# Performance work log

Hardware: AMD Instinct MI355X
Metric: run time of the kernel (lower is better)

Reference implementation:

```python
import jax, jax.numpy as jnp
import numpy as np

C_IN = 128
C_OUT = 128
N_EDGE_TYPE = 7
N_NODE_TYPE = 7
AVG_DEGREE = 7
NUMD = 524288                 # nodes at depth d (multiple of 8)
LNUMD = 32768                 # leaf nodes at depth d-1
NNUM_DM1 = LNUMD + NUMD // 8  # 98304 nodes at depth d-1
PREFIX = 16384                # nodes at depths < d-1 kept in x
N_TOTAL_X = PREFIX + LNUMD + NUMD   # 573440
N_CONV = PREFIX + NNUM_DM1          # 114688 nodes seen by GraphConv
N_EDGES = N_CONV * AVG_DEGREE       # 802816


def setup_inputs() -> dict:
    key = jax.random.key(0)
    ks = jax.random.split(key, 6)
    x = jax.random.normal(ks[0], (N_TOTAL_X, C_IN), dtype=jnp.float32)
    # exactly LNUMD True entries (98304 = 3 * 32768), deterministic
    leaf_mask = (jnp.arange(NNUM_DM1) % 3) == 0
    edge_index = jax.random.randint(ks[1], (2, N_EDGES), 0, N_CONV)
    edge_type = jax.random.randint(ks[2], (N_EDGES,), 0, N_EDGE_TYPE)
    node_type = jax.random.randint(ks[3], (N_CONV,), 0, N_NODE_TYPE)
    w_down = jax.random.normal(ks[4], (C_IN, C_IN, 8), dtype=jnp.float32) * 0.02
    w_conv = jax.random.normal(
        ks[5], (N_EDGE_TYPE * (C_IN + N_NODE_TYPE), C_OUT), dtype=jnp.float32) * 0.02
    return dict(x=x, leaf_mask=leaf_mask, edge_index=edge_index,
                edge_type=edge_type, node_type=node_type,
                w_down=w_down, w_conv=w_conv)


def _graph_conv(x, edge_index, edge_type, node_type, w_conv):
    # x: [N, C]; augment with one-hot node type (n_node_type > 1)
    one_hot = jax.nn.one_hot(node_type, N_NODE_TYPE, dtype=x.dtype)
    xa = jnp.concatenate([x, one_hot], axis=1)          # [N, C+T]
    row, col = edge_index[0], edge_index[1]
    bucket = row * N_EDGE_TYPE + edge_type              # [E]
    # scatter-add neighbor features into per-(node, edge_type) buckets
    col_data = jax.ops.segment_sum(xa[col], bucket,
                                   num_segments=x.shape[0] * N_EDGE_TYPE)
    # [N, n_edge_type*(C+T)] @ [n_edge_type*(C+T), C_out]
    return col_data.reshape(x.shape[0], -1) @ w_conv


def reference(x, leaf_mask, edge_index, edge_type, node_type, w_down, w_conv):
    # Downsample: merge groups of 8 child nodes with a (C, C*8) weight
    xd = x[-NUMD:].reshape(-1, C_IN * 8)                # [NUMD/8, C*8]
    outd = xd @ w_down.reshape(C_IN, C_IN * 8).T        # [NUMD/8, C]
    # Masked scatter assembly: out[leaf_mask] = leaf feats, out[~mask] = outd
    x_leaf = x[-LNUMD - NUMD:-NUMD]                     # [LNUMD, C]
    li = jnp.cumsum(leaf_mask) - 1                      # position among leaves
    ni = jnp.cumsum(~leaf_mask) - 1                     # position among non-leaves
    merged = jnp.where(leaf_mask[:, None], x_leaf[li], outd[ni])  # [NNUM_DM1, C]
    out = jnp.concatenate([x[:-NUMD - LNUMD], merged], axis=0)    # [N_CONV, C]
    return _graph_conv(out, edge_index, edge_type, node_type, w_conv)
```

## Files before the change

kernel.cpp:

```cpp
#include <hip/hip_runtime.h>
#include <stdint.h>

#define C_IN 128
#define NUMD 524288
#define LNUMD 32768
#define NNUM_DM1 (LNUMD + NUMD/8)
#define PREFIX 16384
#define N_CONV (PREFIX + NNUM_DM1)
#define N_EDGES (N_CONV * 7)
#define ND8 (NUMD/8)
#define CAP 32
#define EG 12

#define COPY_BLK ((PREFIX+LNUMD)*32/256)
#define PREPW_N (114688 + 6272 + 131072)
#define PREPW_BLK ((PREPW_N + 255)/256)
#define ZERO_BLK 308
#define DOWN_BLK (ND8/128)
#define SCAT_BLK (N_EDGES/512)

typedef __attribute__((ext_vector_type(8))) short short8;
typedef __attribute__((ext_vector_type(4))) float f32x4;

__device__ inline ushort f2b(float f){
  union { float f; uint32_t u; } v; v.f = f;
  uint32_t r = v.u + 0x7fffu + ((v.u >> 16) & 1u);
  return (ushort)(r >> 16);
}
__device__ inline float b2f_lo(uint32_t u){ union { uint32_t u; float f; } v; v.u = u << 16; return v.f; }
__device__ inline float b2f_hi(uint32_t u){ union { uint32_t u; float f; } v; v.u = u & 0xffff0000u; return v.f; }

#define BAR_LGKM() do { \
    asm volatile("s_waitcnt lgkmcnt(0)" ::: "memory"); \
    __builtin_amdgcn_s_barrier(); \
    asm volatile("" ::: "memory"); \
  } while(0)

__global__ void k_prep(const float* __restrict__ x, const float* __restrict__ wconv,
                       const float* __restrict__ wdown,
                       ushort* __restrict__ xconv, ushort* __restrict__ w16y,
                       ushort* __restrict__ wbias, ushort* __restrict__ wd16,
                       int* __restrict__ cnt){
  const int bid = blockIdx.x;
  if (bid < COPY_BLK){
    int gid = bid*256 + threadIdx.x;
    int row = gid >> 5, seg = (gid & 31) * 4;
    int srow, drow;
    if (row < PREFIX){ srow = row; drow = row; }
    else { int k = row - PREFIX; srow = PREFIX + k; drow = PREFIX + 3*k; }
    const float4 f = *(const float4*)(x + (size_t)srow*C_IN + seg);
    ushort4 o; o.x=f2b(f.x); o.y=f2b(f.y); o.z=f2b(f.z); o.w=f2b(f.w);
    *(ushort4*)(xconv + (size_t)drow*C_IN + seg) = o;
  } else if (bid < COPY_BLK + PREPW_BLK){
    int gid = (bid - COPY_BLK)*256 + threadIdx.x;
    if (gid < 114688){
      int t = gid >> 14, rem = gid & 16383;
      int o = rem >> 7, k = rem & 127;
      w16y[gid] = f2b(wconv[(size_t)(t*135 + k)*128 + o]);
    } else if (gid < 120960){
      int q = gid - 114688;
      int t = q / 896, rem = q % 896;
      int n = rem >> 7, o = rem & 127;
      wbias[q] = f2b(wconv[(size_t)(t*135 + 128 + n)*128 + o]);
    } else if (gid < PREPW_N){
      int i = gid - 120960;
      wd16[i] = f2b(wdown[i]);
    }
  } else {
    int gid = (bid - COPY_BLK - PREPW_BLK)*256 + threadIdx.x;
    int4 z = {0,0,0,0};
    *(int4*)(cnt + gid*4) = z;
  }
}

__global__ __launch_bounds__(512) void k_sd(const int* __restrict__ ei, const int* __restrict__ et,
    int* __restrict__ cnt, int* __restrict__ bucket, unsigned char* __restrict__ used,
    const float* __restrict__ x, const ushort* __restrict__ wd16, ushort* __restrict__ xconv){
  const int bid = blockIdx.x;
  if (bid >= DOWN_BLK){
    int e = (bid - DOWN_BLK)*512 + threadIdx.x;
    int r = ei[e], c = ei[N_EDGES + e], t = et[e];
    int key = c*7 + t;
    int pos = atomicAdd(&cnt[r], 1);
    if (pos < CAP) bucket[r*CAP + pos] = key;
    used[key] = 1;
    return;
  }
  __shared__ ushort As[128*128];
  const int tid = threadIdx.x;
  const int n0 = bid * 128;
  const float* xd = x + (size_t)(PREFIX+LNUMD)*C_IN;

  const int srow = tid >> 2, kbase = (tid & 3) * 32;
  const float* src = xd + (size_t)(n0+srow)*1024 + kbase;

  const int w = tid >> 6, l = tid & 63;
  const int mg = w >> 2, nc = w & 3;
  const int arow = l & 15, kgrp = l >> 4;
  const int obase = nc*32 + arow;

  f32x4 acc[4][2];
  #pragma unroll
  for (int mf=0;mf<4;mf++){ acc[mf][0]=(f32x4){0,0,0,0}; acc[mf][1]=(f32x4){0,0,0,0}; }

  float4 pf[8];
  #pragma unroll
  for (int i=0;i<8;i++) pf[i] = *(const float4*)(src + i*4);

  for (int c = 0; c < 8; ++c){
    #pragma unroll
    for (int i=0;i<4;i++){
      uint4 pk;
      pk.x = (uint)f2b(pf[2*i].x)   | ((uint)f2b(pf[2*i].y)<<16);
      pk.y = (uint)f2b(pf[2*i].z)   | ((uint)f2b(pf[2*i].w)<<16);
      pk.z = (uint)f2b(pf[2*i+1].x) | ((uint)f2b(pf[2*i+1].y)<<16);
      pk.w = (uint)f2b(pf[2*i+1].z) | ((uint)f2b(pf[2*i+1].w)<<16);
      int slot = (kbase >> 3) + i;
      *(uint4*)&As[srow*128 + ((slot ^ ((srow & 7) << 1)) << 3)] = pk;
    }
    BAR_LGKM();

    short8 breg[8];
    #pragma unroll
    for (int kf=0;kf<4;kf++){
      const ushort* bp = wd16 + c*128 + kf*32 + kgrp*8;
      breg[kf*2]   = *(const short8*)(bp + (size_t)obase*1024);
      breg[kf*2+1] = *(const short8*)(bp + (size_t)(obase+16)*1024);
    }
    __builtin_amdgcn_sched_barrier(0);
    if (c < 7){
      const float* s2 = src + (c+1)*128;
      #pragma unroll
      for (int i=0;i<8;i++) pf[i] = *(const float4*)(s2 + i*4);
    }
    __builtin_amdgcn_sched_barrier(0);

    #pragma unroll
    for (int kf=0;kf<4;kf++){
      #pragma unroll
      for (int mf=0;mf<4;mf++){
        int row = mg*64 + mf*16 + arow;
        int slot = (kf*4 + kgrp) ^ ((arow & 7) << 1);
        short8 a = *(const short8*)&As[row*128 + (slot << 3)];
        acc[mf][0] = __builtin_amdgcn_mfma_f32_16x16x32_bf16(a, breg[kf*2],   acc[mf][0], 0,0,0);
        acc[mf][1] = __builtin_amdgcn_mfma_f32_16x16x32_bf16(a, breg[kf*2+1], acc[mf][1], 0,0,0);
      }
    }
    BAR_LGKM();
  }

  #pragma unroll
  for (int mf = 0; mf < 4; ++mf){
    #pragma unroll
    for (int j = 0; j < 4; ++j){
      int rl = mg*64 + mf*16 + (l>>4)*4 + j;
      int n = n0 + rl;
      int i = 3*(n>>1) + 1 + (n&1);
      ushort* dst = xconv + (size_t)(PREFIX + i)*C_IN;
      dst[obase]      = f2b(acc[mf][0][j]);
      dst[obase + 16] = f2b(acc[mf][1][j]);
    }
  }
}

__global__ __launch_bounds__(512) void k_y(const ushort* __restrict__ xconv,
    const ushort* __restrict__ w16y, const ushort* __restrict__ wbias,
    const int* __restrict__ ntype, const unsigned char* __restrict__ used,
    ushort* __restrict__ Y){
  __shared__ ushort As[128*128];
  __shared__ ushort bsh[6272];
  __shared__ int nts[128];
  __shared__ uint usedw[224];
  const int tid = threadIdx.x;
  const int tile = blockIdx.x;
  const unsigned char* usedb = (const unsigned char*)usedw;

  {
    int row = tid >> 2;
    int c0 = (tid & 3) * 4;
    const ushort* src = xconv + ((size_t)tile*128 + row)*128;
    #pragma unroll
    for (int i=0;i<4;i++){
      int c16 = c0 + i;
      uint4 v = *(const uint4*)(src + c16*8);
      *(uint4*)&As[row*128 + ((c16 ^ (row & 7))*8)] = v;
    }
  }
  for (int i = tid; i < 3136; i += 512) ((uint*)bsh)[i] = ((const uint*)wbias)[i];
  if (tid < 128) nts[tid] = ntype[tile*128 + tid];
  if (tid < 224) usedw[tid] = ((const uint*)(used + (size_t)tile*896))[tid];
  __syncthreads();

  const int w = tid >> 6, l = tid & 63;
  const int mg = w >> 2, nc = w & 3;
  const int arow = l & 15, kgrp = l >> 4;
  const int obase = nc*32 + arow;

  for (int t = 0; t < 7; ++t){
    f32x4 acc[4][2];
    #pragma unroll
    for (int mf=0;mf<4;mf++){ acc[mf][0]=(f32x4){0,0,0,0}; acc[mf][1]=(f32x4){0,0,0,0}; }
    const ushort* wt = w16y + t*16384;
    #pragma unroll
    for (int kf = 0; kf < 4; ++kf){
      const int kof = kf*32 + kgrp*8;
      short8 b0 = *(const short8*)(wt + (size_t)obase*128 + kof);
      short8 b1 = *(const short8*)(wt + (size_t)(obase+16)*128 + kof);
      #pragma unroll
      for (int mf = 0; mf < 4; ++mf){
        int row = mg*64 + mf*16 + arow;
        int c16 = (kf*4 + kgrp) ^ (row & 7);
        short8 a = *(const short8*)&As[row*128 + c16*8];
        acc[mf][0] = __builtin_amdgcn_mfma_f32_16x16x32_bf16(a, b0, acc[mf][0], 0,0,0);
        acc[mf][1] = __builtin_amdgcn_mfma_f32_16x16x32_bf16(a, b1, acc[mf][1], 0,0,0);
      }
    }
    #pragma unroll
    for (int mf = 0; mf < 4; ++mf){
      #pragma unroll
      for (int j = 0; j < 4; ++j){
        int rl = mg*64 + mf*16 + (l>>4)*4 + j;
        if (usedb[rl*7 + t]){
          int ntv = nts[rl];
          size_t grow = ((size_t)(tile*128 + rl)*7 + t)*128;
          int bb = (t*7 + ntv)*128;
          Y[grow + obase]      = f2b(acc[mf][0][j] + b2f_lo((uint)bsh[bb + obase]));
          Y[grow + obase + 16] = f2b(acc[mf][1][j] + b2f_lo((uint)bsh[bb + obase + 16]));
        }
      }
    }
  }
}

__global__ __launch_bounds__(256) void k_gather(const int* __restrict__ cnt,
    const int* __restrict__ bucket, const ushort* __restrict__ Y, float* __restrict__ out){
  const int tid = threadIdx.x;
  const int slot = tid >> 4, lane = tid & 15;
  const int v = blockIdx.x*16 + slot;
  const int n = min(cnt[v], CAP);
  const int* brow = bucket + (size_t)v*CAP;
  float acc[8] = {0.f,0.f,0.f,0.f,0.f,0.f,0.f,0.f};

  int m[EG]; uint4 d[EG];
  const int nb = min(n, EG);
  #pragma unroll
  for (int i=0;i<EG;i++) if (i < nb) m[i] = brow[i];
  #pragma unroll
  for (int i=0;i<EG;i++) if (i < nb)
    d[i] = *(const uint4*)(Y + (size_t)m[i]*C_IN + lane*8);
  #pragma unroll
  for (int i=0;i<EG;i++){
    if (i < nb){
      acc[0] += b2f_lo(d[i].x); acc[1] += b2f_hi(d[i].x);
      acc[2] += b2f_lo(d[i].y); acc[3] += b2f_hi(d[i].y);
      acc[4] += b2f_lo(d[i].z); acc[5] += b2f_hi(d[i].z);
      acc[6] += b2f_lo(d[i].w); acc[7] += b2f_hi(d[i].w);
    }
  }
  for (int e = EG; e < n; e += 4){
    int n4 = min(n - e, 4);
    int m4[4]; uint4 d4[4];
    #pragma unroll
    for (int i=0;i<4;i++) if (i < n4) m4[i] = brow[e + i];
    #pragma unroll
    for (int i=0;i<4;i++) if (i < n4)
      d4[i] = *(const uint4*)(Y + (size_t)m4[i]*C_IN + lane*8);
    #pragma unroll
    for (int i=0;i<4;i++){
      if (i < n4){
        acc[0] += b2f_lo(d4[i].x); acc[1] += b2f_hi(d4[i].x);
        acc[2] += b2f_lo(d4[i].y); acc[3] += b2f_hi(d4[i].y);
        acc[4] += b2f_lo(d4[i].z); acc[5] += b2f_hi(d4[i].z);
        acc[6] += b2f_lo(d4[i].w); acc[7] += b2f_hi(d4[i].w);
      }
    }
  }
  float4 o0; o0.x=acc[0]; o0.y=acc[1]; o0.z=acc[2]; o0.w=acc[3];
  float4 o1; o1.x=acc[4]; o1.y=acc[5]; o1.z=acc[6]; o1.w=acc[7];
  float* dst = out + (size_t)v*C_IN + lane*8;
  *(float4*)dst = o0;
  *(float4*)(dst + 4) = o1;
}

extern "C" void kernel_launch(void* const* d_in, const int* in_sizes, int n_in,
                              void* d_out, int out_size, void* d_ws, size_t ws_size,
                              hipStream_t stream){
  const float* x     = (const float*)d_in[0];
  const int*   ei    = (const int*)d_in[2];
  const int*   et    = (const int*)d_in[3];
  const int*   nt    = (const int*)d_in[4];
  const float* wdown = (const float*)d_in[5];
  const float* wconv = (const float*)d_in[6];
  float* out = (float*)d_out;

  char* p = (char*)d_ws;
  ushort* xconv = (ushort*)p; p += (size_t)N_CONV*C_IN*2;
  ushort* wd16  = (ushort*)p; p += (size_t)128*1024*2;
  ushort* w16y  = (ushort*)p; p += (size_t)114688*2;
  ushort* wbias = (ushort*)p; p += 16384;
  int* cnt      = (int*)p;    p += (size_t)N_CONV*4;
  unsigned char* used = (unsigned char*)p; p += 802816;
  int* bucket   = (int*)p;    p += (size_t)N_CONV*CAP*4;
  ushort* Y     = (ushort*)p;

  k_prep<<<COPY_BLK + PREPW_BLK + ZERO_BLK, 256, 0, stream>>>(x, wconv, wdown, xconv, w16y, wbias, wd16, cnt);
  k_sd<<<DOWN_BLK + SCAT_BLK, 512, 0, stream>>>(ei, et, cnt, bucket, used, x, wd16, xconv);
  k_y<<<N_CONV/128, 512, 0, stream>>>(xconv, w16y, wbias, nt, used, Y);
  k_gather<<<N_CONV/16, 256, 0, stream>>>(cnt, bucket, Y, out);
}
```

Before: 289.0 us.

## Fuse per-edge-type Y projection into downsample GEMM and permute node indexing

The downsample GEMM kernel now keeps its bf16 output tile in LDS and immediately multiplies it by the seven per-edge-type conv weights, writing Y directly instead of writing xconv rows for k_y to reload. Nodes are renumbered so that prefix and leaf rows sit contiguously first and downsampled rows after them. Edge keys and node-type lookups are remapped to match, and k_y now only processes the prefix and leaf rows. This removes the xconv write and re-read round trip for the downsampled rows. In exchange the fused blocks carry more LDS and a longer serial tail, and they skip the used-bucket check that k_y applies, so they compute all seven edge types for every row.

```diff
diff --git a/kernel.cpp b/kernel.cpp
--- a/kernel.cpp
+++ b/kernel.cpp
@@ -9,10 +9,11 @@
 #define N_CONV (PREFIX + NNUM_DM1)
 #define N_EDGES (N_CONV * 7)
 #define ND8 (NUMD/8)
+#define NPL (PREFIX + LNUMD)
 #define CAP 32
 #define EG 12
 
-#define COPY_BLK ((PREFIX+LNUMD)*32/256)
+#define COPY_BLK (NPL*32/256)
 #define PREPW_N (114688 + 6272 + 131072)
 #define PREPW_BLK ((PREPW_N + 255)/256)
 #define ZERO_BLK 308
@@ -45,12 +46,9 @@
   if (bid < COPY_BLK){
     int gid = bid*256 + threadIdx.x;
     int row = gid >> 5, seg = (gid & 31) * 4;
-    int srow, drow;
-    if (row < PREFIX){ srow = row; drow = row; }
-    else { int k = row - PREFIX; srow = PREFIX + k; drow = PREFIX + 3*k; }
-    const float4 f = *(const float4*)(x + (size_t)srow*C_IN + seg);
+    const float4 f = *(const float4*)(x + (size_t)row*C_IN + seg);
     ushort4 o; o.x=f2b(f.x); o.y=f2b(f.y); o.z=f2b(f.z); o.w=f2b(f.w);
-    *(ushort4*)(xconv + (size_t)drow*C_IN + seg) = o;
+    *(ushort4*)(xconv + (size_t)row*C_IN + seg) = o;
   } else if (bid < COPY_BLK + PREPW_BLK){
     int gid = (bid - COPY_BLK)*256 + threadIdx.x;
     if (gid < 114688){
@@ -75,21 +73,29 @@
 
 __global__ __launch_bounds__(512) void k_sd(const int* __restrict__ ei, const int* __restrict__ et,
     int* __restrict__ cnt, int* __restrict__ bucket, unsigned char* __restrict__ used,
-    const float* __restrict__ x, const ushort* __restrict__ wd16, ushort* __restrict__ xconv){
+    const float* __restrict__ x, const ushort* __restrict__ wd16,
+    const ushort* __restrict__ w16y, const ushort* __restrict__ wbias,
+    const int* __restrict__ ntype, ushort* __restrict__ Y){
   const int bid = blockIdx.x;
   if (bid >= DOWN_BLK){
     int e = (bid - DOWN_BLK)*512 + threadIdx.x;
     int r = ei[e], c = ei[N_EDGES + e], t = et[e];
-    int key = c*7 + t;
+    int pc;
+    if (c < PREFIX) pc = c;
+    else { int d = c - PREFIX; int q = d/3; int rr = d - q*3;
+           pc = (rr == 0) ? PREFIX + q : NPL + 2*q + (rr-1); }
+    int key = pc*7 + t;
     int pos = atomicAdd(&cnt[r], 1);
     if (pos < CAP) bucket[r*CAP + pos] = key;
     used[key] = 1;
     return;
   }
-  __shared__ ushort As[128*128];
+  __shared__ ushort As[16384];
+  __shared__ ushort bshs[6272];
+  __shared__ int nts[128];
   const int tid = threadIdx.x;
   const int n0 = bid * 128;
-  const float* xd = x + (size_t)(PREFIX+LNUMD)*C_IN;
+  const float* xd = x + (size_t)NPL*C_IN;
 
   const int srow = tid >> 2, kbase = (tid & 3) * 32;
   const float* src = xd + (size_t)(n0+srow)*1024 + kbase;
@@ -98,6 +104,12 @@
   const int mg = w >> 2, nc = w & 3;
   const int arow = l & 15, kgrp = l >> 4;
   const int obase = nc*32 + arow;
+
+  for (int i = tid; i < 3136; i += 512) ((uint*)bshs)[i] = ((const uint*)wbias)[i];
+  if (tid < 128){
+    int n = n0 + tid;
+    nts[tid] = ntype[PREFIX + 3*(n>>1) + 1 + (n&1)];
+  }
 
   f32x4 acc[4][2];
   #pragma unroll
@@ -119,7 +131,6 @@
       *(uint4*)&As[srow*128 + ((slot ^ ((srow & 7) << 1)) << 3)] = pk;
     }
     BAR_LGKM();
-
     short8 breg[8];
     #pragma unroll
     for (int kf=0;kf<4;kf++){
@@ -134,7 +145,6 @@
       for (int i=0;i<8;i++) pf[i] = *(const float4*)(s2 + i*4);
     }
     __builtin_amdgcn_sched_barrier(0);
-
     #pragma unroll
     for (int kf=0;kf<4;kf++){
       #pragma unroll
@@ -152,13 +162,45 @@
   #pragma unroll
   for (int mf = 0; mf < 4; ++mf){
     #pragma unroll
-    for (int j = 0; j < 4; ++j){
-      int rl = mg*64 + mf*16 + (l>>4)*4 + j;
-      int n = n0 + rl;
-      int i = 3*(n>>1) + 1 + (n&1);
-      ushort* dst = xconv + (size_t)(PREFIX + i)*C_IN;
-      dst[obase]      = f2b(acc[mf][0][j]);
-      dst[obase + 16] = f2b(acc[mf][1][j]);
+    for (int side = 0; side < 2; ++side){
+      int col = obase + side*16;
+      int u = col >> 3;
+      #pragma unroll
+      for (int j = 0; j < 4; ++j){
+        int row = mg*64 + mf*16 + kgrp*4 + j;
+        As[row*128 + ((u ^ ((row & 7) << 1)) << 3) + (arow & 7)] = f2b(acc[mf][side][j]);
+      }
+    }
+  }
+  BAR_LGKM();
+
+  const size_t yb = (size_t)NPL + n0;
+  for (int t = 0; t < 7; ++t){
+    const ushort* wt = w16y + t*16384;
+    f32x4 ay[8];
+    #pragma unroll
+    for (int s=0;s<8;s++) ay[s] = (f32x4){0.f,0.f,0.f,0.f};
+    #pragma unroll
+    for (int kf = 0; kf < 4; ++kf){
+      int row = 16*w + arow;
+      int u = (kf*4 + kgrp) ^ ((row & 7) << 1);
+      short8 a = *(const short8*)&As[row*128 + (u << 3)];
+      #pragma unroll
+      for (int s = 0; s < 8; ++s){
+        short8 b = *(const short8*)(wt + (size_t)(s*16 + arow)*128 + kf*32 + kgrp*8);
+        ay[s] = __builtin_amdgcn_mfma_f32_16x16x32_bf16(a, b, ay[s], 0,0,0);
+      }
+    }
+    #pragma unroll
+    for (int s = 0; s < 8; ++s){
+      int col = s*16 + arow;
+      #pragma unroll
+      for (int j = 0; j < 4; ++j){
+        int rl = 16*w + kgrp*4 + j;
+        int ntv = nts[rl];
+        Y[((yb + rl)*7 + t)*128 + col] =
+          f2b(ay[s][j] + b2f_lo((uint)bshs[(t*7 + ntv)*128 + col]));
+      }
     }
   }
 }
@@ -187,7 +229,10 @@
     }
   }
   for (int i = tid; i < 3136; i += 512) ((uint*)bsh)[i] = ((const uint*)wbias)[i];
-  if (tid < 128) nts[tid] = ntype[tile*128 + tid];
+  if (tid < 128){
+    int g = tile*128 + tid;
+    nts[tid] = ntype[g < PREFIX ? g : PREFIX + 3*(g - PREFIX)];
+  }
   if (tid < 224) usedw[tid] = ((const uint*)(used + (size_t)tile*896))[tid];
   __syncthreads();
 
@@ -304,7 +349,7 @@
   ushort* Y     = (ushort*)p;
 
   k_prep<<<COPY_BLK + PREPW_BLK + ZERO_BLK, 256, 0, stream>>>(x, wconv, wdown, xconv, w16y, wbias, wd16, cnt);
-  k_sd<<<DOWN_BLK + SCAT_BLK, 512, 0, stream>>>(ei, et, cnt, bucket, used, x, wd16, xconv);
-  k_y<<<N_CONV/128, 512, 0, stream>>>(xconv, w16y, wbias, nt, used, Y);
+  k_sd<<<DOWN_BLK + SCAT_BLK, 512, 0, stream>>>(ei, et, cnt, bucket, used, x, wd16, w16y, wbias, nt, Y);
+  k_y<<<NPL/128, 512, 0, stream>>>(xconv, w16y, wbias, nt, used, Y);
   k_gather<<<N_CONV/16, 256, 0, stream>>>(cnt, bucket, Y, out);
 }
```

After: 336.6 us. 1.16x slower.
